# Optimization experiments

Measured on AMD Instinct MI355X. Metric: run time of the kernel, lower is better.

The kernel has to match this reference:

```python
import jax, jax.numpy as jnp
import numpy as np

B, N_OBJ, N_ATTR = 8, 10000, 2000
IN_DIM, OUT_DIM, ATTR_DIM = 256, 256, 128
E = 800000


def setup_inputs() -> dict:
    key = jax.random.key(0)
    ks = jax.random.split(key, 10)
    object_feats = jax.random.normal(ks[0], (B, N_OBJ, IN_DIM), dtype=jnp.float32)
    attr_feats = jax.random.normal(ks[1], (B, N_ATTR, ATTR_DIM), dtype=jnp.float32)
    src_obj = jax.random.randint(ks[2], (E,), 0, B * N_OBJ)
    src_attr = jax.random.randint(ks[3], (E,), 0, B * N_ATTR)
    edge_index = jnp.stack([src_obj, src_attr], axis=0)  # [2, E]
    edge_weight = jax.random.uniform(ks[4], (E,), dtype=jnp.float32)
    s = 0.02
    W_a2o = jax.random.normal(ks[5], (IN_DIM, ATTR_DIM), dtype=jnp.float32) * s
    b_a2o = jnp.zeros((IN_DIM,), dtype=jnp.float32)
    W_proj = jax.random.normal(ks[6], (OUT_DIM, IN_DIM), dtype=jnp.float32) * s
    b_proj = jnp.zeros((OUT_DIM,), dtype=jnp.float32)
    W_upd = jax.random.normal(ks[7], (OUT_DIM, IN_DIM + OUT_DIM), dtype=jnp.float32) * s
    b_upd = jnp.zeros((OUT_DIM,), dtype=jnp.float32)
    return {
        "object_feats": object_feats,
        "attr_feats": attr_feats,
        "edge_index": edge_index,
        "edge_weight": edge_weight,
        "W_a2o": W_a2o, "b_a2o": b_a2o,
        "W_proj": W_proj, "b_proj": b_proj,
        "W_upd": W_upd, "b_upd": b_upd,
    }


def reference(object_feats, attr_feats, edge_index, edge_weight,
              W_a2o, b_a2o, W_proj, b_proj, W_upd, b_upd):
    bsz, num_objects, in_dim = object_feats.shape
    flat_objects = object_feats.reshape(bsz * num_objects, in_dim)
    flat_attrs = attr_feats.reshape(bsz * attr_feats.shape[1], -1)
    src_obj = edge_index[0]
    src_attr = edge_index[1]
    # gather attr rows, apply linear: [E, in_dim]
    attr_msgs = flat_attrs[src_attr] @ W_a2o.T + b_a2o
    weighted_msgs = attr_msgs * edge_weight[:, None]
    # weighted scatter-add into object slots
    agg = jax.ops.segment_sum(weighted_msgs, src_obj, num_segments=bsz * num_objects)
    weight_sums = jax.ops.segment_sum(edge_weight, src_obj, num_segments=bsz * num_objects)
    agg = agg / jnp.clip(weight_sums, 1e-6)[:, None]
    proj_msgs = agg @ W_proj.T + b_proj
    combined = jnp.concatenate([flat_objects, proj_msgs], axis=-1)
    updated = jax.nn.relu(combined @ W_upd.T + b_upd)  # dropout=0 (eval)
    return updated.reshape(bsz, num_objects, -1)
```

## Files before the change

kernel.cpp:

```cpp
#include <hip/hip_runtime.h>
#include <hip/hip_bf16.h>

#define BSZ      8
#define NOBJ     10000
#define NATTR    2000
#define IN_DIM   256
#define OUT_DIM  256
#define ATTR_DIM 128
#define E_NUM    800000
#define M_ROWS   (BSZ * NOBJ)
#define K_TOT    (IN_DIM + ATTR_DIM)

#define SCAN_CHUNK 1024
#define SCAN_NBLK  ((M_ROWS + SCAN_CHUNK - 1) / SCAN_CHUNK)

typedef short bf16x8 __attribute__((ext_vector_type(8)));
typedef float f32x4  __attribute__((ext_vector_type(4)));

__device__ __forceinline__ short f2bf(float f) {
    union { float f; unsigned u; } v; v.f = f;
    unsigned r = v.u + 0x7FFFu + ((v.u >> 16) & 1u);
    return (short)(r >> 16);
}
__device__ __forceinline__ unsigned pack_bf2(float x, float y) {
    return ((unsigned)(unsigned short)f2bf(x)) | (((unsigned)(unsigned short)f2bf(y)) << 16);
}

__device__ __forceinline__ int wfrag_idx(int n, int k) {
    return (((k >> 5) * 16 + (n >> 4)) * 64 + ((k >> 3) & 3) * 16 + (n & 15)) * 8 + (k & 7);
}

__global__ void prep1(const float* __restrict__ W_upd, const float* __restrict__ W_proj,
                      float* __restrict__ M1) {
    int i = blockIdx.x;
    int j = threadIdx.x;
    const float* wrow = W_upd + i * 512 + 256;
    float acc = 0.f;
    for (int k = 0; k < 256; ++k) acc += wrow[k] * W_proj[k * 256 + j];
    M1[i * 256 + j] = acc;
}

__global__ void prep2(const float* __restrict__ W_upd, const float* __restrict__ W_a2o,
                      const float* __restrict__ b_a2o, const float* __restrict__ b_proj,
                      const float* __restrict__ b_upd, const float* __restrict__ M1,
                      unsigned short* __restrict__ Wfrag, float* __restrict__ v1,
                      float* __restrict__ v2) {
    int i = blockIdx.x;
    int j = threadIdx.x;
    const float* m1row = M1 + i * 256;
    float acc = 0.f;
    for (int k = 0; k < 256; ++k) acc += m1row[k] * W_a2o[k * 128 + j];
    Wfrag[wfrag_idx(i, 256 + j)] = (unsigned short)f2bf(acc);
    Wfrag[wfrag_idx(i, j)]       = (unsigned short)f2bf(W_upd[i * 512 + j]);
    Wfrag[wfrag_idx(i, 128 + j)] = (unsigned short)f2bf(W_upd[i * 512 + 128 + j]);

    __shared__ float r1[128], r2[128];
    r1[j] = m1row[j] * b_a2o[j] + m1row[j + 128] * b_a2o[j + 128];
    r2[j] = W_upd[i * 512 + 256 + j] * b_proj[j] +
            W_upd[i * 512 + 256 + 128 + j] * b_proj[j + 128];
    __syncthreads();
    for (int s = 64; s > 0; s >>= 1) {
        if (j < s) { r1[j] += r1[j + s]; r2[j] += r2[j + s]; }
        __syncthreads();
    }
    if (j == 0) { v1[i] = r1[0]; v2[i] = r2[0] + b_upd[i]; }
}

__global__ void conv_attrs(const float* __restrict__ attrs, unsigned int* __restrict__ attrs_bf) {
    int i = blockIdx.x * blockDim.x + threadIdx.x;
    float2 v = *reinterpret_cast<const float2*>(attrs + (size_t)i * 2);
    attrs_bf[i] = pack_bf2(v.x, v.y);
}

__global__ void hist_kernel(const int* __restrict__ ei, int* __restrict__ count) {
    int e = blockIdx.x * blockDim.x + threadIdx.x;
    if (e < E_NUM) atomicAdd(&count[ei[e]], 1);
}

__global__ void scan_partial(const int* __restrict__ count, int* __restrict__ blockSums) {
    __shared__ int sh[256];
    int t = threadIdx.x;
    int base = blockIdx.x * SCAN_CHUNK + t * 4;
    int s = 0;
    if (base + 3 < M_ROWS) {
        int4 v = *reinterpret_cast<const int4*>(count + base);
        s = v.x + v.y + v.z + v.w;
    } else {
        for (int i = 0; i < 4; ++i) if (base + i < M_ROWS) s += count[base + i];
    }
    sh[t] = s;
    __syncthreads();
    for (int off = 128; off > 0; off >>= 1) {
        if (t < off) sh[t] += sh[t + off];
        __syncthreads();
    }
    if (t == 0) blockSums[blockIdx.x] = sh[0];
}

__global__ void scan_sums(const int* __restrict__ blockSums, int* __restrict__ blockOffsets) {
    __shared__ int sh[128];
    int t = threadIdx.x;
    int v = (t < SCAN_NBLK) ? blockSums[t] : 0;
    sh[t] = v;
    __syncthreads();
    for (int off = 1; off < 128; off <<= 1) {
        int u = (t >= off) ? sh[t - off] : 0;
        __syncthreads();
        sh[t] += u;
        __syncthreads();
    }
    if (t < SCAN_NBLK) blockOffsets[t] = sh[t] - v;
}

__global__ void scan_final(const int* __restrict__ count, const int* __restrict__ blockOffsets,
                           int* __restrict__ start, int* __restrict__ cursor) {
    __shared__ int sh[256];
    int t = threadIdx.x;
    int base = blockIdx.x * SCAN_CHUNK + t * 4;
    int c0 = 0, c1 = 0, c2 = 0, c3 = 0;
    if (base + 3 < M_ROWS) {
        int4 v = *reinterpret_cast<const int4*>(count + base);
        c0 = v.x; c1 = v.y; c2 = v.z; c3 = v.w;
    } else {
        if (base + 0 < M_ROWS) c0 = count[base + 0];
        if (base + 1 < M_ROWS) c1 = count[base + 1];
        if (base + 2 < M_ROWS) c2 = count[base + 2];
        if (base + 3 < M_ROWS) c3 = count[base + 3];
    }
    int s = c0 + c1 + c2 + c3;
    sh[t] = s;
    __syncthreads();
    for (int off = 1; off < 256; off <<= 1) {
        int u = (t >= off) ? sh[t - off] : 0;
        __syncthreads();
        sh[t] += u;
        __syncthreads();
    }
    int run = blockOffsets[blockIdx.x] + sh[t] - s;
    if (base + 0 < M_ROWS) { start[base + 0] = run; cursor[base + 0] = run; run += c0; }
    if (base + 1 < M_ROWS) { start[base + 1] = run; cursor[base + 1] = run; run += c1; }
    if (base + 2 < M_ROWS) { start[base + 2] = run; cursor[base + 2] = run; run += c2; }
    if (base + 3 < M_ROWS) { start[base + 3] = run; cursor[base + 3] = run; run += c3; }
    if (blockIdx.x == 0 && t == 0) start[M_ROWS] = E_NUM;
}

__global__ void scatter_kernel(const int* __restrict__ ei, const float* __restrict__ ew,
                               int* __restrict__ cursor, int2* __restrict__ s_edge) {
    int e = blockIdx.x * blockDim.x + threadIdx.x;
    if (e < E_NUM) {
        int o = ei[e];
        int pos = atomicAdd(&cursor[o], 1);
        s_edge[pos] = make_int2(ei[E_NUM + e], __float_as_int(ew[e]));
    }
}

__global__ void __launch_bounds__(256) agg_kernel(const unsigned int* __restrict__ attrs_bf,
        const int* __restrict__ start, const int2* __restrict__ s_edge,
        unsigned int* __restrict__ nrm, float* __restrict__ s_out) {
    int wave = (int)((blockIdx.x * blockDim.x + threadIdx.x) >> 6);
    int lane = threadIdx.x & 63;
    if (wave >= M_ROWS) return;
    int beg = start[wave], end = start[wave + 1];
    float a0 = 0.f, a1 = 0.f, ws = 0.f;
    if (beg < end) {
        int last = end - 1;
        int2 e[8];
#pragma unroll
        for (int k = 0; k < 8; ++k) e[k] = s_edge[min(beg + k, last)];
        for (int j = beg; j < end; j += 8) {
            unsigned u[8];
            float w[8];
#pragma unroll
            for (int k = 0; k < 8; ++k) {
                u[k] = attrs_bf[e[k].x * 64 + lane];
                w[k] = (j + k < end) ? __int_as_float(e[k].y) : 0.f;
            }
            int jn = j + 8;
            if (jn < end) {
#pragma unroll
                for (int k = 0; k < 8; ++k) e[k] = s_edge[min(jn + k, last)];
            }
#pragma unroll
            for (int k = 0; k < 8; ++k) {
                a0 += w[k] * __uint_as_float(u[k] << 16);
                a1 += w[k] * __uint_as_float(u[k] & 0xFFFF0000u);
                ws += w[k];
            }
        }
    }
    float inv = 1.f / fmaxf(ws, 1e-6f);
    nrm[wave * 64 + lane] = pack_bf2(a0 * inv, a1 * inv);
    if (lane == 0) s_out[wave] = ws * inv;
}

__global__ void __launch_bounds__(256, 2) gemm_out(
    const float* __restrict__ obj, const unsigned short* __restrict__ nrm,
    const bf16x8* __restrict__ Wfrag, const float* __restrict__ v1,
    const float* __restrict__ v2, const float* __restrict__ s_arr,
    float* __restrict__ out) {
    int tid = threadIdx.x;
    int w = tid >> 6, lane = tid & 63;
    int l15 = lane & 15, quad = lane >> 4;
    int m_base = blockIdx.x * 128 + w * 32;

    f32x4 acc[2][16];
#pragma unroll
    for (int a = 0; a < 2; ++a)
#pragma unroll
        for (int b = 0; b < 16; ++b) acc[a][b] = (f32x4){0.f, 0.f, 0.f, 0.f};

    for (int kt = 0; kt < 12; ++kt) {
        int k0 = kt * 32;
        bf16x8 af[2];
#pragma unroll
        for (int mt = 0; mt < 2; ++mt) {
            int m = m_base + mt * 16 + l15;
            if (k0 < 256) {
                const float* p = obj + (size_t)m * 256 + k0 + quad * 8;
                float4 x0 = *reinterpret_cast<const float4*>(p);
                float4 x1 = *reinterpret_cast<const float4*>(p + 4);
                bf16x8 a;
                a[0] = f2bf(x0.x); a[1] = f2bf(x0.y); a[2] = f2bf(x0.z); a[3] = f2bf(x0.w);
                a[4] = f2bf(x1.x); a[5] = f2bf(x1.y); a[6] = f2bf(x1.z); a[7] = f2bf(x1.w);
                af[mt] = a;
            } else {
                af[mt] = *reinterpret_cast<const bf16x8*>(nrm + (size_t)m * 128 + (k0 - 256) + quad * 8);
            }
        }
        const bf16x8* bp = Wfrag + (size_t)(kt * 16) * 64 + lane;
#pragma unroll
        for (int nt = 0; nt < 16; ++nt) {
            bf16x8 bf_ = bp[nt * 64];
            acc[0][nt] = __builtin_amdgcn_mfma_f32_16x16x32_bf16(af[0], bf_, acc[0][nt], 0, 0, 0);
            acc[1][nt] = __builtin_amdgcn_mfma_f32_16x16x32_bf16(af[1], bf_, acc[1][nt], 0, 0, 0);
        }
    }

    float v1v[16], v2v[16];
#pragma unroll
    for (int nt = 0; nt < 16; ++nt) {
        v1v[nt] = v1[nt * 16 + l15];
        v2v[nt] = v2[nt * 16 + l15];
    }
#pragma unroll
    for (int mt = 0; mt < 2; ++mt) {
#pragma unroll
        for (int r = 0; r < 4; ++r) {
            int m = m_base + mt * 16 + quad * 4 + r;
            float sv = s_arr[m];
            float* orow = out + (size_t)m * 256;
#pragma unroll
            for (int nt = 0; nt < 16; ++nt) {
                float val = acc[mt][nt][r] + sv * v1v[nt] + v2v[nt];
                orow[nt * 16 + l15] = fmaxf(val, 0.f);
            }
        }
    }
}

extern "C" void kernel_launch(void* const* d_in, const int* in_sizes, int n_in,
                              void* d_out, int out_size, void* d_ws, size_t ws_size,
                              hipStream_t stream) {
    const float* obj    = (const float*)d_in[0];
    const float* attrs  = (const float*)d_in[1];
    const int*   ei     = (const int*)d_in[2];
    const float* ew     = (const float*)d_in[3];
    const float* W_a2o  = (const float*)d_in[4];
    const float* b_a2o  = (const float*)d_in[5];
    const float* W_proj = (const float*)d_in[6];
    const float* b_proj = (const float*)d_in[7];
    const float* W_upd  = (const float*)d_in[8];
    const float* b_upd  = (const float*)d_in[9];
    float* out = (float*)d_out;
    char* ws = (char*)d_ws;

    unsigned int* nrm      = (unsigned int*)(ws);
    float* s_arr           = (float*)(ws + 20480000);
    int*   count           = (int*)  (ws + 20800000);
    int*   start           = (int*)  (ws + 21120000);
    int*   cursor          = (int*)  (ws + 21440256);
    int2*  s_edge          = (int2*) (ws + 21760256);
    unsigned int* attrs_bf = (unsigned int*)(ws + 28160256);
    float* M1              = (float*)(ws + 32256256);
    unsigned short* Wfrag  = (unsigned short*)(ws + 32518400);
    float* v1              = (float*)(ws + 32715008);
    float* v2              = (float*)(ws + 32716032);
    int* blockSums         = (int*)  (ws + 32256256);
    int* blockOffsets      = (int*)  (ws + 32256256 + 512);

    (void)hipMemsetAsync(count, 0, M_ROWS * sizeof(int), stream);

    prep1<<<256, 256, 0, stream>>>(W_upd, W_proj, M1);
    prep2<<<256, 128, 0, stream>>>(W_upd, W_a2o, b_a2o, b_proj, b_upd, M1, Wfrag, v1, v2);
    conv_attrs<<<(BSZ * NATTR * 64) / 256, 256, 0, stream>>>(attrs, attrs_bf);
    hist_kernel<<<(E_NUM + 255) / 256, 256, 0, stream>>>(ei, count);
    scan_partial<<<SCAN_NBLK, 256, 0, stream>>>(count, blockSums);
    scan_sums<<<1, 128, 0, stream>>>(blockSums, blockOffsets);
    scan_final<<<SCAN_NBLK, 256, 0, stream>>>(count, blockOffsets, start, cursor);
    scatter_kernel<<<(E_NUM + 255) / 256, 256, 0, stream>>>(ei, ew, cursor, s_edge);
    agg_kernel<<<M_ROWS / 4, 256, 0, stream>>>(attrs_bf, start, s_edge, nrm, s_arr);
    gemm_out<<<M_ROWS / 128, 256, 0, stream>>>(obj, (const unsigned short*)nrm,
                                               (const bf16x8*)Wfrag, v1, v2, s_arr, out);
}
```

Measured before the change: 380.1 us.

## Stage weight fragments in double-buffered LDS and split gemm_out tile across N halves

The output GEMM now cooperatively loads the weight fragments for each K-step into a double-buffered shared-memory tile and prefetches the next K-step's A and B operands while the MFMAs for the current step run. Each block covers 64 rows instead of 128, with waves split across the two N halves, so there are twice as many blocks and half the accumulators per wave. Launch bounds go to 3 blocks per CU. The aim is to stop every wave from reloading the full weight matrix out of global or L2 and to hide load latency. In exchange it adds a block barrier per K-step and repeats the A-side loads across the two N-half waves.

```diff
diff --git a/kernel.cpp b/kernel.cpp
--- a/kernel.cpp
+++ b/kernel.cpp
@@ -193,54 +193,79 @@
     if (lane == 0) s_out[wave] = ws * inv;
 }
 
-__global__ void __launch_bounds__(256, 2) gemm_out(
+__global__ void __launch_bounds__(256, 3) gemm_out(
     const float* __restrict__ obj, const unsigned short* __restrict__ nrm,
-    const bf16x8* __restrict__ Wfrag, const float* __restrict__ v1,
+    const int4* __restrict__ Wfrag4, const float* __restrict__ v1,
     const float* __restrict__ v2, const float* __restrict__ s_arr,
     float* __restrict__ out) {
+    __shared__ int4 Bs[2][1024];
+
     int tid = threadIdx.x;
     int w = tid >> 6, lane = tid & 63;
     int l15 = lane & 15, quad = lane >> 4;
-    int m_base = blockIdx.x * 128 + w * 32;
-
-    f32x4 acc[2][16];
+    int nhalf = w & 1, msub = w >> 1;
+    int m_base = blockIdx.x * 64 + msub * 32;
+
+    f32x4 acc[2][8];
 #pragma unroll
     for (int a = 0; a < 2; ++a)
 #pragma unroll
-        for (int b = 0; b < 16; ++b) acc[a][b] = (f32x4){0.f, 0.f, 0.f, 0.f};
+        for (int b = 0; b < 8; ++b) acc[a][b] = (f32x4){0.f, 0.f, 0.f, 0.f};
+
+    int4 q0, q1, q2, q3;
+    bf16x8 af[2], afn[2];
+
+#define FETCH_B(kt) do { const int4* p = Wfrag4 + (kt) * 1024 + tid; \
+        q0 = p[0]; q1 = p[256]; q2 = p[512]; q3 = p[768]; } while (0)
+#define WRITE_B(buf) do { int4* d = &Bs[buf][tid]; \
+        d[0] = q0; d[256] = q1; d[512] = q2; d[768] = q3; } while (0)
+#define LOAD_A(kt, dst) do { int k0_ = (kt) * 32; \
+        _Pragma("unroll") \
+        for (int mt = 0; mt < 2; ++mt) { \
+            int m_ = m_base + mt * 16 + l15; \
+            if (k0_ < 256) { \
+                const float* p_ = obj + (size_t)m_ * 256 + k0_ + quad * 8; \
+                float4 x0 = *reinterpret_cast<const float4*>(p_); \
+                float4 x1 = *reinterpret_cast<const float4*>(p_ + 4); \
+                bf16x8 a_; \
+                a_[0] = f2bf(x0.x); a_[1] = f2bf(x0.y); a_[2] = f2bf(x0.z); a_[3] = f2bf(x0.w); \
+                a_[4] = f2bf(x1.x); a_[5] = f2bf(x1.y); a_[6] = f2bf(x1.z); a_[7] = f2bf(x1.w); \
+                (dst)[mt] = a_; \
+            } else { \
+                (dst)[mt] = *reinterpret_cast<const bf16x8*>(nrm + (size_t)m_ * 128 + (k0_ - 256) + quad * 8); \
+            } \
+        } } while (0)
+
+    FETCH_B(0);
+    LOAD_A(0, af);
+    WRITE_B(0);
 
     for (int kt = 0; kt < 12; ++kt) {
-        int k0 = kt * 32;
-        bf16x8 af[2];
-#pragma unroll
-        for (int mt = 0; mt < 2; ++mt) {
-            int m = m_base + mt * 16 + l15;
-            if (k0 < 256) {
-                const float* p = obj + (size_t)m * 256 + k0 + quad * 8;
-                float4 x0 = *reinterpret_cast<const float4*>(p);
-                float4 x1 = *reinterpret_cast<const float4*>(p + 4);
-                bf16x8 a;
-                a[0] = f2bf(x0.x); a[1] = f2bf(x0.y); a[2] = f2bf(x0.z); a[3] = f2bf(x0.w);
-                a[4] = f2bf(x1.x); a[5] = f2bf(x1.y); a[6] = f2bf(x1.z); a[7] = f2bf(x1.w);
-                af[mt] = a;
-            } else {
-                af[mt] = *reinterpret_cast<const bf16x8*>(nrm + (size_t)m * 128 + (k0 - 256) + quad * 8);
-            }
-        }
-        const bf16x8* bp = Wfrag + (size_t)(kt * 16) * 64 + lane;
-#pragma unroll
-        for (int nt = 0; nt < 16; ++nt) {
-            bf16x8 bf_ = bp[nt * 64];
-            acc[0][nt] = __builtin_amdgcn_mfma_f32_16x16x32_bf16(af[0], bf_, acc[0][nt], 0, 0, 0);
-            acc[1][nt] = __builtin_amdgcn_mfma_f32_16x16x32_bf16(af[1], bf_, acc[1][nt], 0, 0, 0);
-        }
-    }
-
-    float v1v[16], v2v[16];
-#pragma unroll
-    for (int nt = 0; nt < 16; ++nt) {
-        v1v[nt] = v1[nt * 16 + l15];
-        v2v[nt] = v2[nt * 16 + l15];
+        int cur = kt & 1;
+        __syncthreads();
+        if (kt < 11) {
+            FETCH_B(kt + 1);
+            LOAD_A(kt + 1, afn);
+        }
+        const bf16x8* bp = reinterpret_cast<const bf16x8*>(&Bs[cur][0]) + nhalf * 8 * 64 + lane;
+#pragma unroll
+        for (int nt = 0; nt < 8; ++nt) {
+            bf16x8 b = bp[nt * 64];
+            acc[0][nt] = __builtin_amdgcn_mfma_f32_16x16x32_bf16(af[0], b, acc[0][nt], 0, 0, 0);
+            acc[1][nt] = __builtin_amdgcn_mfma_f32_16x16x32_bf16(af[1], b, acc[1][nt], 0, 0, 0);
+        }
+        if (kt < 11) {
+            WRITE_B(cur ^ 1);
+            af[0] = afn[0]; af[1] = afn[1];
+        }
+    }
+
+    float v1v[8], v2v[8];
+#pragma unroll
+    for (int nt = 0; nt < 8; ++nt) {
+        int col = nhalf * 128 + nt * 16 + l15;
+        v1v[nt] = v1[col];
+        v2v[nt] = v2[col];
     }
 #pragma unroll
     for (int mt = 0; mt < 2; ++mt) {
@@ -248,14 +273,17 @@
         for (int r = 0; r < 4; ++r) {
             int m = m_base + mt * 16 + quad * 4 + r;
             float sv = s_arr[m];
-            float* orow = out + (size_t)m * 256;
-#pragma unroll
-            for (int nt = 0; nt < 16; ++nt) {
+            float* orow = out + (size_t)m * 256 + nhalf * 128;
+#pragma unroll
+            for (int nt = 0; nt < 8; ++nt) {
                 float val = acc[mt][nt][r] + sv * v1v[nt] + v2v[nt];
                 orow[nt * 16 + l15] = fmaxf(val, 0.f);
             }
         }
     }
+#undef FETCH_B
+#undef WRITE_B
+#undef LOAD_A
 }
 
 extern "C" void kernel_launch(void* const* d_in, const int* in_sizes, int n_in,
@@ -299,6 +327,6 @@
     scan_final<<<SCAN_NBLK, 256, 0, stream>>>(count, blockOffsets, start, cursor);
     scatter_kernel<<<(E_NUM + 255) / 256, 256, 0, stream>>>(ei, ew, cursor, s_edge);
     agg_kernel<<<M_ROWS / 4, 256, 0, stream>>>(attrs_bf, start, s_edge, nrm, s_arr);
-    gemm_out<<<M_ROWS / 128, 256, 0, stream>>>(obj, (const unsigned short*)nrm,
-                                               (const bf16x8*)Wfrag, v1, v2, s_arr, out);
-}
+    gemm_out<<<M_ROWS / 64, 256, 0, stream>>>(obj, (const unsigned short*)nrm,
+                                              (const int4*)Wfrag, v1, v2, s_arr, out);
+}
```

Result: faster. 356.2 us (-6.3%).
